# Performance work log

Hardware: AMD Instinct MI355X
Metric: run time of the kernel (lower is better)

Reference implementation:

```python
import jax, jax.numpy as jnp
import numpy as np

D_MODEL = 768
N_HEADS = 12
HEAD_DIM = D_MODEL // N_HEADS


def setup_inputs() -> dict:
    key = jax.random.key(0)
    ks = jax.random.split(key, 9)
    s = 0.02
    B, S = 16, 1024
    return {
        "x": jax.random.normal(ks[0], (B, S, D_MODEL), dtype=jnp.float32),
        "Wq": jax.random.normal(ks[1], (D_MODEL, D_MODEL), dtype=jnp.float32) * s,
        "bq": jnp.zeros((D_MODEL,), dtype=jnp.float32),
        "Wk": jax.random.normal(ks[2], (D_MODEL, D_MODEL), dtype=jnp.float32) * s,
        "bk": jnp.zeros((D_MODEL,), dtype=jnp.float32),
        "Wv": jax.random.normal(ks[3], (D_MODEL, D_MODEL), dtype=jnp.float32) * s,
        "bv": jnp.zeros((D_MODEL,), dtype=jnp.float32),
        "Wc": jax.random.normal(ks[4], (D_MODEL, D_MODEL), dtype=jnp.float32) * s,
        "bc": jnpp if False else jnp.zeros((D_MODEL,), dtype=jnp.float32),
    }


def _split_heads(t):
    # [B, S, D] -> [B, H, S, Dh]
    B, S, _ = t.shape
    return t.reshape(B, S, N_HEADS, HEAD_DIM).transpose(0, 2, 1, 3)


def reference(x, Wq, bq, Wk, bk, Wv, bv, Wc, bc):
    # nn.Linear: y = x @ W.T + b ; here W stored as [out, in]-equivalent square
    q = _split_heads(x @ Wq.T + bq)
    k = _split_heads(x @ Wk.T + bk)
    v = _split_heads(x @ Wv.T + bv)
    scale = jnp.asarray(HEAD_DIM, x.dtype) ** 0.5
    scores = jnp.einsum("bhsd,bhtd->bhst", q, k) / scale  # [B,H,S,S]
    attn = jax.nn.softmax(scores, axis=-1)
    # dropout omitted (deterministic / inference-mode reference)
    ctx = jnp.einsum("bhst,bhtd->bhsd", attn, v)  # [B,H,S,Dh]
    B, H, S, Dh = ctx.shape
    ctx = ctx.transpose(0, 2, 1, 3).reshape(B, S, H * Dh)
    return ctx @ Wc.T + bc
```

## Files before the change

kernel.cpp:

```cpp
#include <hip/hip_runtime.h>
#include <hip/hip_bf16.h>
#include <stdint.h>

#define D_MODEL 768
#define NHEADS 12
#define HDIM 64
#define BATCH 16
#define SEQ 1024
#define MTOK (BATCH*SEQ)
#define LOG2E 1.4426950408889634f

typedef __bf16 bfrag  __attribute__((ext_vector_type(8)));
typedef __bf16 bf16x4 __attribute__((ext_vector_type(4)));
typedef float  f32x4  __attribute__((ext_vector_type(4)));

__device__ __forceinline__ void gload16(const void* g, void* l) {
  __builtin_amdgcn_global_load_lds(
      (const __attribute__((address_space(1))) unsigned int*)g,
      (__attribute__((address_space(3))) unsigned int*)l, 16, 0, 0);
}

__global__ __launch_bounds__(256) void convert_kernel(
    const float* __restrict__ x,
    const float* __restrict__ Wq, const float* __restrict__ Wk,
    const float* __restrict__ Wv, const float* __restrict__ Wc,
    __bf16* __restrict__ xb, __bf16* __restrict__ Wb)
{
  const size_t NX = (size_t)MTOK * D_MODEL;
  const size_t NW = (size_t)D_MODEL * D_MODEL;
  size_t i = ((size_t)blockIdx.x * 256 + threadIdx.x) * 4;
  const float* src; __bf16* dst; size_t off;
  if (i < NX) { src = x; dst = xb; off = i; }
  else {
    size_t wj = i - NX;
    int which = (int)(wj / NW);
    off = wj - (size_t)which * NW;
    src = which == 0 ? Wq : which == 1 ? Wk : which == 2 ? Wv : Wc;
    dst = Wb + (size_t)which * NW;
  }
  f32x4 v = *(const f32x4*)(src + off);
  bf16x4 o;
  o[0] = (__bf16)v[0]; o[1] = (__bf16)v[1]; o[2] = (__bf16)v[2]; o[3] = (__bf16)v[3];
  *(bf16x4*)(dst + off) = o;
}

__global__ __launch_bounds__(256) void qkv_gemm(
    const __bf16* __restrict__ A,
    const __bf16* __restrict__ W,
    const float* __restrict__ bq, const float* __restrict__ bk, const float* __restrict__ bv,
    __bf16* __restrict__ Qb,
    __bf16* __restrict__ Kb,
    __bf16* __restrict__ VTb)
{
  __shared__ __bf16 As[128 * 32];
  __shared__ __bf16 Bs[128 * 32];
  const int tid = threadIdx.x;
  const int lane = tid & 63, w = tid >> 6;
  const int wm = w >> 1, wn = w & 1;
  const int bm = blockIdx.x, bn = blockIdx.y;
  const int r4 = lane >> 2, c8 = (lane & 3) << 3;
  const int l15 = lane & 15, q8 = (lane >> 4) << 3;

  f32x4 acc[4][4];
#pragma unroll
  for (int mt = 0; mt < 4; ++mt)
#pragma unroll
    for (int nt = 0; nt < 4; ++nt) acc[mt][nt] = (f32x4){0.f, 0.f, 0.f, 0.f};

  const size_t am0 = (size_t)bm * 128;
  const size_t bn0 = (size_t)bn * 128;

  for (int kt = 0; kt < 24; ++kt) {
    const int k0 = kt * 32;
#pragma unroll
    for (int i = 0; i < 2; ++i) {
      const int rr = i * 64 + w * 16;
      gload16(A + (am0 + rr + r4) * D_MODEL + k0 + c8, &As[rr * 32]);
      gload16(W + (bn0 + rr + r4) * D_MODEL + k0 + c8, &Bs[rr * 32]);
    }
    __syncthreads();
    bfrag af[4], bf[4];
#pragma unroll
    for (int t = 0; t < 4; ++t) {
      af[t] = *(const bfrag*)&As[(wm * 64 + t * 16 + l15) * 32 + q8];
      bf[t] = *(const bfrag*)&Bs[(wn * 64 + t * 16 + l15) * 32 + q8];
    }
#pragma unroll
    for (int mt = 0; mt < 4; ++mt)
#pragma unroll
      for (int nt = 0; nt < 4; ++nt)
        acc[mt][nt] = __builtin_amdgcn_mfma_f32_16x16x32_bf16(af[mt], bf[nt], acc[mt][nt], 0, 0, 0);
    __syncthreads();
  }

  const int which = bn / 6;
  const int obase = (bn % 6) * 128 + wn * 64;
  const float* bias = which == 0 ? bq : which == 1 ? bk : bv;
  const float qscale = 0.125f * LOG2E;
#pragma unroll
  for (int mt = 0; mt < 4; ++mt) {
    const int row0 = bm * 128 + wm * 64 + mt * 16 + (lane >> 4) * 4;
    const int b = row0 >> 10, s = row0 & 1023;
#pragma unroll
    for (int nt = 0; nt < 4; ++nt) {
      const int o = obase + nt * 16 + l15;
      const float bo = bias[o];
      const int h = o >> 6, d = o & 63;
      const size_t hb = ((size_t)(b * NHEADS + h)) << 16;
      if (which == 2) {
        bf16x4 pv;
#pragma unroll
        for (int r = 0; r < 4; ++r) pv[r] = (__bf16)(acc[mt][nt][r] + bo);
        *(bf16x4*)&VTb[hb + ((size_t)d << 10) + s] = pv;
      } else if (which == 0) {
#pragma unroll
        for (int r = 0; r < 4; ++r)
          Qb[hb + ((size_t)(s + r) << 6) + d] = (__bf16)((acc[mt][nt][r] + bo) * qscale);
      } else {
#pragma unroll
        for (int r = 0; r < 4; ++r)
          Kb[hb + ((size_t)(s + r) << 6) + d] = (__bf16)(acc[mt][nt][r] + bo);
      }
    }
  }
}

__global__ __launch_bounds__(256, 4) void attn_kernel(
    const __bf16* __restrict__ Qb, const __bf16* __restrict__ Kb,
    const __bf16* __restrict__ VTb, __bf16* __restrict__ ctx)
{
  __shared__ __bf16 Qs[64][72];
  __shared__ __bf16 Ks[64][72];
  __shared__ __bf16 VTs[64][72];
  __shared__ __bf16 Ps[64][72];
  const int tid = threadIdx.x, lane = tid & 63, w = tid >> 6;
  const int qt = blockIdx.x, bh = blockIdx.y;
  const int l15 = lane & 15, quad = lane >> 4, q8 = quad << 3;
  const size_t base = (size_t)bh << 16;

  const int srow = tid >> 3, scol = (tid & 7) << 3;

#pragma unroll
  for (int i = 0; i < 2; ++i) {
    int row = i * 32 + srow;
    *(uint4*)&Qs[row][scol] = *(const uint4*)(Qb + base + (size_t)(qt * 64 + row) * 64 + scol);
  }
  __syncthreads();

  bfrag bq0 = *(const bfrag*)&Qs[w * 16 + l15][q8];
  bfrag bq1 = *(const bfrag*)&Qs[w * 16 + l15][32 + q8];

  f32x4 Oa[4];
  float lsum = 0.f;
#pragma unroll
  for (int nt = 0; nt < 4; ++nt) Oa[nt] = (f32x4){0.f, 0.f, 0.f, 0.f};

  for (int j = 0; j < 16; ++j) {
    uint4 k0 = *(const uint4*)(Kb  + base + (size_t)(j * 64 + srow) * 64 + scol);
    uint4 k1 = *(const uint4*)(Kb  + base + (size_t)(j * 64 + 32 + srow) * 64 + scol);
    uint4 v0 = *(const uint4*)(VTb + base + (size_t)srow * 1024 + j * 64 + scol);
    uint4 v1 = *(const uint4*)(VTb + base + (size_t)(32 + srow) * 1024 + j * 64 + scol);
    __syncthreads();
    *(uint4*)&Ks[srow][scol]       = k0;
    *(uint4*)&Ks[32 + srow][scol]  = k1;
    *(uint4*)&VTs[srow][scol]      = v0;
    *(uint4*)&VTs[32 + srow][scol] = v1;
    __syncthreads();

#pragma unroll
    for (int tt = 0; tt < 4; ++tt) {
      bfrag ak0 = *(const bfrag*)&Ks[tt * 16 + l15][q8];
      bfrag ak1 = *(const bfrag*)&Ks[tt * 16 + l15][32 + q8];
      f32x4 s = (f32x4){0.f, 0.f, 0.f, 0.f};
      s = __builtin_amdgcn_mfma_f32_16x16x32_bf16(ak0, bq0, s, 0, 0, 0);
      s = __builtin_amdgcn_mfma_f32_16x16x32_bf16(ak1, bq1, s, 0, 0, 0);
      bf16x4 p4;
#pragma unroll
      for (int r = 0; r < 4; ++r) {
        float p = exp2f(s[r]);
        lsum += p;
        p4[r] = (__bf16)p;
      }
      *(bf16x4*)&Ps[w * 16 + l15][tt * 16 + quad * 4] = p4;
    }

    bfrag bp0 = *(const bfrag*)&Ps[w * 16 + l15][q8];
    bfrag bp1 = *(const bfrag*)&Ps[w * 16 + l15][32 + q8];
#pragma unroll
    for (int nt = 0; nt < 4; ++nt) {
      bfrag av0 = *(const bfrag*)&VTs[nt * 16 + l15][q8];
      bfrag av1 = *(const bfrag*)&VTs[nt * 16 + l15][32 + q8];
      Oa[nt] = __builtin_amdgcn_mfma_f32_16x16x32_bf16(av0, bp0, Oa[nt], 0, 0, 0);
      Oa[nt] = __builtin_amdgcn_mfma_f32_16x16x32_bf16(av1, bp1, Oa[nt], 0, 0, 0);
    }
  }

  lsum += __shfl_xor(lsum, 16);
  lsum += __shfl_xor(lsum, 32);
  const float inv = 1.0f / lsum;

  const int b = bh / NHEADS, h = bh - b * NHEADS;
  const int s = qt * 64 + w * 16 + l15;
  const size_t rowbase = ((size_t)(b * SEQ + s)) * D_MODEL + h * HDIM;
#pragma unroll
  for (int nt = 0; nt < 4; ++nt) {
    bf16x4 o4;
#pragma unroll
    for (int r = 0; r < 4; ++r) o4[r] = (__bf16)(Oa[nt][r] * inv);
    *(bf16x4*)&ctx[rowbase + nt * 16 + quad * 4] = o4;
  }
}

__global__ __launch_bounds__(256) void out_gemm(
    const __bf16* __restrict__ A,
    const __bf16* __restrict__ W,
    const float* __restrict__ bc,
    float* __restrict__ out)
{
  __shared__ __bf16 As[128 * 32];
  __shared__ __bf16 Bs[128 * 32];
  const int tid = threadIdx.x;
  const int lane = tid & 63, w = tid >> 6;
  const int wm = w >> 1, wn = w & 1;
  const int bm = blockIdx.x, bn = blockIdx.y;
  const int r4 = lane >> 2, c8 = (lane & 3) << 3;
  const int l15 = lane & 15, q8 = (lane >> 4) << 3;

  f32x4 acc[4][4];
#pragma unroll
  for (int mt = 0; mt < 4; ++mt)
#pragma unroll
    for (int nt = 0; nt < 4; ++nt) acc[mt][nt] = (f32x4){0.f, 0.f, 0.f, 0.f};

  const size_t am0 = (size_t)bm * 128;
  const size_t bn0 = (size_t)bn * 128;

  for (int kt = 0; kt < 24; ++kt) {
    const int k0 = kt * 32;
#pragma unroll
    for (int i = 0; i < 2; ++i) {
      const int rr = i * 64 + w * 16;
      gload16(A + (am0 + rr + r4) * D_MODEL + k0 + c8, &As[rr * 32]);
      gload16(W + (bn0 + rr + r4) * D_MODEL + k0 + c8, &Bs[rr * 32]);
    }
    __syncthreads();
    bfrag af[4], bf[4];
#pragma unroll
    for (int t = 0; t < 4; ++t) {
      af[t] = *(const bfrag*)&As[(wm * 64 + t * 16 + l15) * 32 + q8];
      bf[t] = *(const bfrag*)&Bs[(wn * 64 + t * 16 + l15) * 32 + q8];
    }
#pragma unroll
    for (int mt = 0; mt < 4; ++mt)
#pragma unroll
      for (int nt = 0; nt < 4; ++nt)
        acc[mt][nt] = __builtin_amdgcn_mfma_f32_16x16x32_bf16(af[mt], bf[nt], acc[mt][nt], 0, 0, 0);
    __syncthreads();
  }

#pragma unroll
  for (int mt = 0; mt < 4; ++mt) {
    const int row0 = bm * 128 + wm * 64 + mt * 16 + (lane >> 4) * 4;
#pragma unroll
    for (int nt = 0; nt < 4; ++nt) {
      const int o = bn * 128 + wn * 64 + nt * 16 + l15;
      const float bo = bc[o];
#pragma unroll
      for (int r = 0; r < 4; ++r)
        out[(size_t)(row0 + r) * D_MODEL + o] = acc[mt][nt][r] + bo;
    }
  }
}

extern "C" void kernel_launch(void* const* d_in, const int* in_sizes, int n_in,
                              void* d_out, int out_size, void* d_ws, size_t ws_size,
                              hipStream_t stream)
{
  const float* x  = (const float*)d_in[0];
  const float* Wq = (const float*)d_in[1];
  const float* bq = (const float*)d_in[2];
  const float* Wk = (const float*)d_in[3];
  const float* bk = (const float*)d_in[4];
  const float* Wv = (const float*)d_in[5];
  const float* bv = (const float*)d_in[6];
  const float* Wc = (const float*)d_in[7];
  const float* bc = (const float*)d_in[8];
  float* out = (float*)d_out;

  char* ws = (char*)d_ws;
  __bf16* xb  = (__bf16*)(ws);
  __bf16* Wb  = (__bf16*)(ws + 25165824);
  __bf16* Qb  = (__bf16*)(ws + 29884416);
  __bf16* Kb  = (__bf16*)(ws + 55050240);
  __bf16* VTb = (__bf16*)(ws + 80216064);
  __bf16* ctx = xb;

  convert_kernel<<<14592, 256, 0, stream>>>(x, Wq, Wk, Wv, Wc, xb, Wb);
  qkv_gemm<<<dim3(128, 18), 256, 0, stream>>>(xb, Wb, bq, bk, bv, Qb, Kb, VTb);
  attn_kernel<<<dim3(16, 192), 256, 0, stream>>>(Qb, Kb, VTb, ctx);
  out_gemm<<<dim3(128, 6), 256, 0, stream>>>(ctx, Wb + 3 * 589824, bc, out);
}
```

Before: 310.6 us.

## Pre-tile and XOR-swizzle Q/K/V layouts, double-buffer attention loads via direct-to-LDS

```diff
diff --git a/kernel.cpp b/kernel.cpp
--- a/kernel.cpp
+++ b/kernel.cpp
@@ -111,15 +111,24 @@
         bf16x4 pv;
 #pragma unroll
         for (int r = 0; r < 4; ++r) pv[r] = (__bf16)(acc[mt][nt][r] + bo);
-        *(bf16x4*)&VTb[hb + ((size_t)d << 10) + s] = pv;
+        const int tc = s & 63;
+        const size_t addr = hb + (size_t)(s >> 6) * 4096 + (size_t)d * 64
+                          + (size_t)((((tc >> 3) ^ (d & 7))) << 3) + (tc & 7);
+        *(bf16x4*)&VTb[addr] = pv;
       } else if (which == 0) {
 #pragma unroll
-        for (int r = 0; r < 4; ++r)
-          Qb[hb + ((size_t)(s + r) << 6) + d] = (__bf16)((acc[mt][nt][r] + bo) * qscale);
+        for (int r = 0; r < 4; ++r) {
+          const int sr = s + r;
+          const size_t addr = hb + (size_t)sr * 64 + (size_t)(((d >> 3) ^ (sr & 7)) << 3) + (d & 7);
+          Qb[addr] = (__bf16)((acc[mt][nt][r] + bo) * qscale);
+        }
       } else {
 #pragma unroll
-        for (int r = 0; r < 4; ++r)
-          Kb[hb + ((size_t)(s + r) << 6) + d] = (__bf16)(acc[mt][nt][r] + bo);
+        for (int r = 0; r < 4; ++r) {
+          const int sr = s + r;
+          const size_t addr = hb + (size_t)sr * 64 + (size_t)(((d >> 3) ^ (sr & 7)) << 3) + (d & 7);
+          Kb[addr] = (__bf16)(acc[mt][nt][r] + bo);
+        }
       }
     }
   }
@@ -129,26 +138,33 @@
     const __bf16* __restrict__ Qb, const __bf16* __restrict__ Kb,
     const __bf16* __restrict__ VTb, __bf16* __restrict__ ctx)
 {
-  __shared__ __bf16 Qs[64][72];
-  __shared__ __bf16 Ks[64][72];
-  __shared__ __bf16 VTs[64][72];
-  __shared__ __bf16 Ps[64][72];
+  __shared__ __bf16 Ks[2][4096];
+  __shared__ __bf16 VTs[2][4096];
+  __shared__ __bf16 Ps[4096];
   const int tid = threadIdx.x, lane = tid & 63, w = tid >> 6;
   const int qt = blockIdx.x, bh = blockIdx.y;
-  const int l15 = lane & 15, quad = lane >> 4, q8 = quad << 3;
+  const int l15 = lane & 15, quad = lane >> 4;
+  const int h3 = l15 & 7;
   const size_t base = (size_t)bh << 16;
 
-  const int srow = tid >> 3, scol = (tid & 7) << 3;
-
-#pragma unroll
-  for (int i = 0; i < 2; ++i) {
-    int row = i * 32 + srow;
-    *(uint4*)&Qs[row][scol] = *(const uint4*)(Qb + base + (size_t)(qt * 64 + row) * 64 + scol);
+  const int soff = w * 1024 + lane * 8;
+
+  {
+    const __bf16* gq = Qb + base + qt * 4096 + soff;
+    const __bf16* gk = Kb + base + soff;
+    const __bf16* gv = VTb + base + soff;
+    gload16(gq,       &Ps[soff]);
+    gload16(gq + 512, &Ps[soff + 512]);
+    gload16(gk,       &Ks[0][soff]);
+    gload16(gk + 512, &Ks[0][soff + 512]);
+    gload16(gv,       &VTs[0][soff]);
+    gload16(gv + 512, &VTs[0][soff + 512]);
   }
   __syncthreads();
 
-  bfrag bq0 = *(const bfrag*)&Qs[w * 16 + l15][q8];
-  bfrag bq1 = *(const bfrag*)&Qs[w * 16 + l15][32 + q8];
+  const int fq = (w * 16 + l15) * 64 + ((quad ^ h3) << 3);
+  bfrag bq0 = *(const bfrag*)&Ps[fq];
+  bfrag bq1 = *(const bfrag*)&Ps[fq ^ 32];
 
   f32x4 Oa[4];
   float lsum = 0.f;
@@ -156,43 +172,47 @@
   for (int nt = 0; nt < 4; ++nt) Oa[nt] = (f32x4){0.f, 0.f, 0.f, 0.f};
 
   for (int j = 0; j < 16; ++j) {
-    uint4 k0 = *(const uint4*)(Kb  + base + (size_t)(j * 64 + srow) * 64 + scol);
-    uint4 k1 = *(const uint4*)(Kb  + base + (size_t)(j * 64 + 32 + srow) * 64 + scol);
-    uint4 v0 = *(const uint4*)(VTb + base + (size_t)srow * 1024 + j * 64 + scol);
-    uint4 v1 = *(const uint4*)(VTb + base + (size_t)(32 + srow) * 1024 + j * 64 + scol);
-    __syncthreads();
-    *(uint4*)&Ks[srow][scol]       = k0;
-    *(uint4*)&Ks[32 + srow][scol]  = k1;
-    *(uint4*)&VTs[srow][scol]      = v0;
-    *(uint4*)&VTs[32 + srow][scol] = v1;
-    __syncthreads();
+    const int cb = j & 1, nb = cb ^ 1;
+    if (j < 15) {
+      const __bf16* gk = Kb + base + (j + 1) * 4096 + soff;
+      const __bf16* gv = VTb + base + (j + 1) * 4096 + soff;
+      gload16(gk,       &Ks[nb][soff]);
+      gload16(gk + 512, &Ks[nb][soff + 512]);
+      gload16(gv,       &VTs[nb][soff]);
+      gload16(gv + 512, &VTs[nb][soff + 512]);
+    }
 
 #pragma unroll
     for (int tt = 0; tt < 4; ++tt) {
-      bfrag ak0 = *(const bfrag*)&Ks[tt * 16 + l15][q8];
-      bfrag ak1 = *(const bfrag*)&Ks[tt * 16 + l15][32 + q8];
-      f32x4 s = (f32x4){0.f, 0.f, 0.f, 0.f};
-      s = __builtin_amdgcn_mfma_f32_16x16x32_bf16(ak0, bq0, s, 0, 0, 0);
-      s = __builtin_amdgcn_mfma_f32_16x16x32_bf16(ak1, bq1, s, 0, 0, 0);
+      const int fk = (tt * 16 + l15) * 64 + ((quad ^ h3) << 3);
+      bfrag ak0 = *(const bfrag*)&Ks[cb][fk];
+      bfrag ak1 = *(const bfrag*)&Ks[cb][fk ^ 32];
+      f32x4 s4 = (f32x4){0.f, 0.f, 0.f, 0.f};
+      s4 = __builtin_amdgcn_mfma_f32_16x16x32_bf16(ak0, bq0, s4, 0, 0, 0);
+      s4 = __builtin_amdgcn_mfma_f32_16x16x32_bf16(ak1, bq1, s4, 0, 0, 0);
       bf16x4 p4;
 #pragma unroll
       for (int r = 0; r < 4; ++r) {
-        float p = exp2f(s[r]);
+        float p = exp2f(s4[r]);
         lsum += p;
         p4[r] = (__bf16)p;
       }
-      *(bf16x4*)&Ps[w * 16 + l15][tt * 16 + quad * 4] = p4;
-    }
-
-    bfrag bp0 = *(const bfrag*)&Ps[w * 16 + l15][q8];
-    bfrag bp1 = *(const bfrag*)&Ps[w * 16 + l15][32 + q8];
+      const int u = 2 * tt + (quad >> 1);
+      *(bf16x4*)&Ps[(w * 16 + l15) * 64 + ((u ^ h3) << 3) + ((quad & 1) << 2)] = p4;
+    }
+
+    const int fp = (w * 16 + l15) * 64 + ((quad ^ h3) << 3);
+    bfrag bp0 = *(const bfrag*)&Ps[fp];
+    bfrag bp1 = *(const bfrag*)&Ps[fp ^ 32];
 #pragma unroll
     for (int nt = 0; nt < 4; ++nt) {
-      bfrag av0 = *(const bfrag*)&VTs[nt * 16 + l15][q8];
-      bfrag av1 = *(const bfrag*)&VTs[nt * 16 + l15][32 + q8];
+      const int fv = (nt * 16 + l15) * 64 + ((quad ^ h3) << 3);
+      bfrag av0 = *(const bfrag*)&VTs[cb][fv];
+      bfrag av1 = *(const bfrag*)&VTs[cb][fv ^ 32];
       Oa[nt] = __builtin_amdgcn_mfma_f32_16x16x32_bf16(av0, bp0, Oa[nt], 0, 0, 0);
       Oa[nt] = __builtin_amdgcn_mfma_f32_16x16x32_bf16(av1, bp1, Oa[nt], 0, 0, 0);
     }
+    __syncthreads();
   }
 
   lsum += __shfl_xor(lsum, 16);
```

Measured after the change: 306.2 us. Within noise of the previous version (-1.4%).
